# Performance work log

Hardware: AMD Instinct MI355X
Metric: run time of the kernel (lower is better)

Reference implementation:

```python
import jax, jax.numpy as jnp
import numpy as np

NUM_EMBEDDINGS = 4096
EMBEDDING_DIM = 256
COMMITMENT_COST = 0.25
N_INPUTS = 32768


def setup_inputs() -> dict:
    key = jax.random.key(0)
    k1, k2 = jax.random.split(key)
    inputs = jax.random.normal(k1, (N_INPUTS, EMBEDDING_DIM), dtype=jnp.float32)
    # embedding.weight initialized uniform(-1/K, 1/K)
    W = jax.random.uniform(k2, (NUM_EMBEDDINGS, EMBEDDING_DIM), dtype=jnp.float32,
                           minval=-1.0 / NUM_EMBEDDINGS, maxval=1.0 / NUM_EMBEDDINGS)
    return {"inputs": inputs, "W": W}


def reference(inputs, W):
    # pairwise squared L2 distances: [N, K]
    distances = (jnp.sum(inputs ** 2, axis=1, keepdims=True)
                 + jnp.sum(W ** 2, axis=1)
                 - 2.0 * inputs @ W.T)
    encoding_indices = jnp.argmin(distances, axis=1)           # [N]
    # one-hot scatter + matmul in torch == direct gather
    quantized = W[encoding_indices]                            # [N, D]

    e_latent_loss = jnp.mean((jax.lax.stop_gradient(quantized) - inputs) ** 2)
    q_latent_loss = jnp.mean((quantized - jax.lax.stop_gradient(inputs)) ** 2)
    loss = q_latent_loss + COMMITMENT_COST * e_latent_loss

    # straight-through estimator
    quantized_st = inputs + jax.lax.stop_gradient(quantized - inputs)

    # avg_probs = mean over N of one-hot encodings == normalized counts
    counts = jnp.zeros((NUM_EMBEDDINGS,), dtype=jnp.float32).at[encoding_indices].add(1.0)
    avg_probs = counts / inputs.shape[0]
    perplexity = jnp.exp(-jnp.sum(avg_probs * jnp.log(avg_probs + 1e-10)))

    return (loss, quantized_st, perplexity)
```

## Files before the change

### kernel.cpp

```cpp
#include <hip/hip_runtime.h>
#include <hip/hip_bf16.h>

#define M_IN  32768
#define K_EMB 4096
#define D_DIM 256

#define BM 256
#define BN 256
#define BK 32

#define WS_HWSQ   0
#define WS_PACKS  16384
#define WS_COUNTS 278528
#define WS_LOSS   294912
#define WS_XSQ    295168

using f32x4  = __attribute__((ext_vector_type(4))) float;
using bf16x8 = __attribute__((ext_vector_type(8))) short;

#define GLL16(g, p) __builtin_amdgcn_global_load_lds( \
    (const __attribute__((address_space(1))) void*)(g), \
    (__attribute__((address_space(3))) void*)(p), 16, 0, 0)

__device__ __forceinline__ unsigned short bf16_rtn(float f) {
    __hip_bfloat16 h = __float2bfloat16(f);
    return *reinterpret_cast<unsigned short*>(&h);
}

__global__ __launch_bounds__(256) void convx_kernel(const float* __restrict__ X,
                                                    unsigned short* __restrict__ Xb,
                                                    float* __restrict__ xsq,
                                                    unsigned long long* __restrict__ packs)
{
    const int l  = threadIdx.x & 63;
    const int wv = threadIdx.x >> 6;
    const int n  = blockIdx.x * 4 + wv;
    float4 v = ((const float4*)(X + (size_t)n * D_DIM))[l];
    float s = v.x * v.x + v.y * v.y + v.z * v.z + v.w * v.w;
    union { unsigned short u[4]; uint2 q; } p;
    p.u[0] = bf16_rtn(v.x); p.u[1] = bf16_rtn(v.y);
    p.u[2] = bf16_rtn(v.z); p.u[3] = bf16_rtn(v.w);
    ((uint2*)(Xb + (size_t)n * D_DIM))[l] = p.q;
#pragma unroll
    for (int off = 32; off; off >>= 1) s += __shfl_xor(s, off);
    if (l == 0) { xsq[n] = s; packs[n] = ~0ull; }
}

__global__ __launch_bounds__(256) void convw_kernel(const float* __restrict__ W,
                                                    unsigned short* __restrict__ Wb,
                                                    float* __restrict__ hwsq,
                                                    int* __restrict__ counts,
                                                    float* __restrict__ loss_slots)
{
    const int l = threadIdx.x & 63;
    const int k = blockIdx.x * 4 + (threadIdx.x >> 6);
    const int g = blockIdx.x * 256 + threadIdx.x;
    if (g < K_EMB) counts[g] = 0;
    if (g < 64)    loss_slots[g] = 0.f;
    float4 v = ((const float4*)(W + (size_t)k * D_DIM))[l];
    float s = v.x * v.x + v.y * v.y + v.z * v.z + v.w * v.w;
    union { unsigned short u[4]; uint2 q; } p;
    p.u[0] = bf16_rtn(v.x); p.u[1] = bf16_rtn(v.y);
    p.u[2] = bf16_rtn(v.z); p.u[3] = bf16_rtn(v.w);
    ((uint2*)(Wb + (size_t)k * D_DIM))[l] = p.q;
#pragma unroll
    for (int off = 32; off; off >>= 1) s += __shfl_xor(s, off);
    if (l == 0) hwsq[k] = 0.5f * s;
}


#define STAGE_A(KT, S) { \
  _Pragma("unroll") \
  for (int j_ = 0; j_ < 2; ++j_) { \
    const int row_ = (j_*8 + w)*16 + (l >> 2); \
    const int ch_  = ((l & 3) ^ ((l >> 3) & 3)); \
    const unsigned short* src_ = Xb + (size_t)(m0 + row_) * D_DIM + (KT)*BK + ch_*8; \
    GLL16(src_, lds + (S)*32768 + (j_*8 + w)*1024); \
  } }

#define STAGE_B(KT, S) { \
  _Pragma("unroll") \
  for (int j_ = 0; j_ < 2; ++j_) { \
    const int row_ = (j_*8 + w)*16 + (l >> 2); \
    const int ch_  = ((l & 3) ^ ((l >> 3) & 3)); \
    const unsigned short* src_ = Wb + (size_t)(nbase + row_) * D_DIM + (KT)*BK + ch_*8; \
    GLL16(src_, lds + (S)*32768 + 16384 + (j_*8 + w)*1024); \
  } }

#define K_ITER(T, VM)                                                          \
  {                                                                            \
    asm volatile("s_waitcnt vmcnt(" #VM ")" ::: "memory");                     \
    __builtin_amdgcn_s_barrier();                                              \
    __builtin_amdgcn_sched_barrier(0);                                         \
    const char* As_ = (const char*)lds + ((T)&3)*32768;                        \
    const char* Bs_ = As_ + 16384;                                             \
    if ((T) < 5) STAGE_A((T)+3, ((T)+3)&3);                                    \
    bf16x8 bfr[4], af[4];                                                      \
    _Pragma("unroll")                                                          \
    for (int nj = 0; nj < 4; nj++)                                             \
      bfr[nj] = *(const bf16x8*)(Bs_ + (rbB + nj*16)*64 + cswz);               \
    _Pragma("unroll")                                                          \
    for (int mi = 0; mi < 4; mi++)                                             \
      af[mi] = *(const bf16x8*)(As_ + (rbA + mi*16)*64 + cswz);                \
    asm volatile("s_waitcnt lgkmcnt(0)" ::: "memory");                         \
    __builtin_amdgcn_sched_barrier(0);                                         \
    __builtin_amdgcn_s_setprio(1);                                             \
    _Pragma("unroll")                                                          \
    for (int mi = 0; mi < 4; mi++)                                             \
      _Pragma("unroll")                                                        \
      for (int nj = 0; nj < 4; nj++)                                           \
        acc[mi][nj] = __builtin_amdgcn_mfma_f32_16x16x32_bf16(                 \
            af[mi], bfr[nj], acc[mi][nj], 0, 0, 0);                            \
    __builtin_amdgcn_s_setprio(0);                                             \
    if ((T) < 5) STAGE_B((T)+3, ((T)+3)&3);                                    \
    _Pragma("unroll")                                                          \
    for (int mi = 0; mi < 4; mi++)                                             \
      af[mi] = *(const bf16x8*)(As_ + (rbA + 64 + mi*16)*64 + cswz);           \
    asm volatile("s_waitcnt lgkmcnt(0)" ::: "memory");                         \
    __builtin_amdgcn_sched_barrier(0);                                         \
    __builtin_amdgcn_s_setprio(1);                                             \
    _Pragma("unroll")                                                          \
    for (int mi = 0; mi < 4; mi++)                                             \
      _Pragma("unroll")                                                        \
      for (int nj = 0; nj < 4; nj++)                                           \
        acc[4+mi][nj] = __builtin_amdgcn_mfma_f32_16x16x32_bf16(               \
            af[mi], bfr[nj], acc[4+mi][nj], 0, 0, 0);                          \
    __builtin_amdgcn_s_setprio(0);                                             \
  }

__global__ __launch_bounds__(512, 2) void dist_kernel(const unsigned short* __restrict__ Xb,
                                                      const unsigned short* __restrict__ Wb,
                                                      const float* __restrict__ hwsq,
                                                      unsigned long long* __restrict__ packs)
{
    __shared__ char lds[131072];

    const int t = threadIdx.x;
    const int l = t & 63;
    const int w = t >> 6;
    const int wm = w >> 2, wn = w & 3;

    const int id  = blockIdx.x;
    const int swz = (id & 7) * 256 + (id >> 3);
    const int nb = swz & 15, mb = swz >> 4;
    const int m0 = mb * BM, nbase = nb * BN;

    const int rbA = wm * 128 + (l & 15);
    const int rbB = wn * 64  + (l & 15);
    const int cswz = ((l >> 4) * 16) ^ (((((l & 15)) >> 1) & 3) << 4);

    f32x4 acc[8][4];
#pragma unroll
    for (int mi = 0; mi < 8; mi++)
#pragma unroll
        for (int nj = 0; nj < 4; nj++) acc[mi][nj] = (f32x4){0.f, 0.f, 0.f, 0.f};

    STAGE_A(0, 0); STAGE_B(0, 0);
    STAGE_A(1, 1); STAGE_B(1, 1);
    STAGE_A(2, 2); STAGE_B(2, 2);

    K_ITER(0, 8)
    K_ITER(1, 8)
    K_ITER(2, 8)
    K_ITER(3, 8)
    K_ITER(4, 8)
    K_ITER(5, 8)
    K_ITER(6, 4)
    K_ITER(7, 0)

    unsigned long long* mlds = (unsigned long long*)lds;
    float hw[4];
#pragma unroll
    for (int nj = 0; nj < 4; nj++)
        hw[nj] = hwsq[nbase + wn * 64 + nj * 16 + (l & 15)];

#pragma unroll
    for (int mi = 0; mi < 8; mi++) {
#pragma unroll
        for (int r = 0; r < 4; r++) {
            float bv = 3.4e38f; int bi = 0;
#pragma unroll
            for (int nj = 0; nj < 4; nj++) {
                const float v = hw[nj] - acc[mi][nj][r];
                const int idx = nbase + wn * 64 + nj * 16 + (l & 15);
                if (v < bv) { bv = v; bi = idx; }
            }
            unsigned long long pk =
                ((unsigned long long)__float_as_uint(bv + 1.0f) << 32) | (unsigned)bi;
#pragma unroll
            for (int off = 1; off < 16; off <<= 1) {
                const unsigned long long o = __shfl_xor(pk, off);
                if (o < pk) pk = o;
            }
            if ((l & 15) == 0)
                mlds[(wm * 128 + mi * 16 + (l >> 4) * 4 + r) * 4 + wn] = pk;
        }
    }
    __syncthreads();
    if (t < BM) {
        unsigned long long p = mlds[t * 4];
#pragma unroll
        for (int q = 1; q < 4; q++) {
            const unsigned long long o = mlds[t * 4 + q];
            if (o < p) p = o;
        }
        atomicMin(&packs[m0 + t], p);
    }
}

__global__ __launch_bounds__(256) void merge_kernel(const float* __restrict__ W,
                                                    const unsigned long long* __restrict__ packs,
                                                    const float* __restrict__ xsq,
                                                    int* __restrict__ counts,
                                                    float* __restrict__ loss_slots,
                                                    char* __restrict__ outbase )
{
    const int l   = threadIdx.x & 63;
    const int wv  = threadIdx.x >> 6;
    const int n0w = blockIdx.x * 64 + wv * 16;

    const unsigned long long pk = packs[n0w + (l & 15)];
    const int pkl = (int)(unsigned)(pk & 0xffffffffull);

    if (l < 16) atomicAdd(&counts[pkl], 1);

    float ls = xsq[n0w + (l & 15)] + 2.0f * (__uint_as_float((unsigned)(pk >> 32)) - 1.0f);
#pragma unroll
    for (int off = 32; off; off >>= 1) ls += __shfl_xor(ls, off);
    if (l == 0) atomicAdd(&loss_slots[(blockIdx.x * 4 + wv) & 63], 0.25f * ls);

    float4 v[16];
#pragma unroll
    for (int r = 0; r < 16; r++) {
        const int idxr = __shfl(pkl, r);
        v[r] = ((const float4*)(W + (size_t)idxr * D_DIM))[l];
    }

#pragma unroll
    for (int r = 0; r < 16; r++) {
        char* bp = outbase + (size_t)(n0w + r) * 1024;
        const float nx = __shfl_down(v[r].x, 1);
        const float ny = __shfl_down(v[r].y, 1);
        const float nz = __shfl_down(v[r].z, 1);
        if (l < 63)
            *(float4*)(bp + 12 + 16 * l) = make_float4(v[r].w, nx, ny, nz);
        if (l == 0) {
            ((float*)bp)[0] = v[r].x; ((float*)bp)[1] = v[r].y; ((float*)bp)[2] = v[r].z;
        }
        if (l == 63) ((float*)bp)[255] = v[r].w;
    }
}

__global__ __launch_bounds__(256) void finalize_kernel(const int* __restrict__ counts,
                                                       const float* __restrict__ loss_slots,
                                                       float* __restrict__ out)
{
    const int tid = threadIdx.x;
    float ent = 0.f;
    for (int k = tid; k < K_EMB; k += 256) {
        const float p = (float)counts[k] * (1.0f / (float)M_IN);
        ent += p * logf(p + 1e-10f);
    }
#pragma unroll
    for (int off = 32; off; off >>= 1) ent += __shfl_xor(ent, off);
    __shared__ float red[4];
    if ((tid & 63) == 0) red[tid >> 6] = ent;
    __syncthreads();
    if (tid == 0) {
        const float e = red[0] + red[1] + red[2] + red[3];
        float ls = 0.f;
        for (int i = 0; i < 64; i++) ls += loss_slots[i];
        out[0] = 1.25f * ls / ((float)M_IN * (float)D_DIM);
        out[1 + (size_t)M_IN * D_DIM] = expf(-e);
    }
}

extern "C" void kernel_launch(void* const* d_in, const int* in_sizes, int n_in,
                              void* d_out, int out_size, void* d_ws, size_t ws_size,
                              hipStream_t stream)
{
    const float* X = (const float*)d_in[0];
    const float* W = (const float*)d_in[1];
    float* out = (float*)d_out;
    char*  ws  = (char*)d_ws;

    float* hwsq               = (float*)(ws + WS_HWSQ);
    unsigned long long* packs = (unsigned long long*)(ws + WS_PACKS);
    int*   counts             = (int*)(ws + WS_COUNTS);
    float* loss_slots         = (float*)(ws + WS_LOSS);
    float* xsq                = (float*)(ws + WS_XSQ);

    unsigned short* Xb = (unsigned short*)((char*)d_out + 16);
    unsigned short* Wb = (unsigned short*)((char*)d_out + 16 + 16777216);

    convx_kernel<<<M_IN / 4, 256, 0, stream>>>(X, Xb, xsq, packs);
    convw_kernel<<<K_EMB / 4, 256, 0, stream>>>(W, Wb, hwsq, counts, loss_slots);
    dist_kernel<<<(M_IN / BM) * (K_EMB / BN), 512, 0, stream>>>(Xb, Wb, hwsq, packs);
    merge_kernel<<<M_IN / 64, 256, 0, stream>>>(W, packs, xsq, counts, loss_slots,
                                                (char*)d_out + 4);
    finalize_kernel<<<1, 256, 0, stream>>>(counts, loss_slots, out);
}
```

Baseline: 244.3 us.

## Keep codebook tile in registers and stream bf16-converted inputs through LDS

Restructures the distance GEMM so that each wave holds a 64-row slice of the bf16 codebook in registers for the whole kernel. Each block walks 1024 input rows, converting fp32 inputs to bf16 on the fly into a double-buffered swizzled LDS tile. This removes the separate input conversion kernel and its bf16 round trip through global memory, and the x-squared norm for the loss is now computed in the merge kernel. The trade-offs are heavy register pressure, only 256 blocks, and more global atomicMin traffic, since each row partial is issued per 16-lane group instead of being reduced in LDS first.

```diff
diff --git a/kernel.cpp b/kernel.cpp
--- a/kernel.cpp
+++ b/kernel.cpp
@@ -4,46 +4,18 @@
 #define M_IN  32768
 #define K_EMB 4096
 #define D_DIM 256
-
-#define BM 256
-#define BN 256
-#define BK 32
 
 #define WS_HWSQ   0
 #define WS_PACKS  16384
 #define WS_COUNTS 278528
 #define WS_LOSS   294912
-#define WS_XSQ    295168
 
 using f32x4  = __attribute__((ext_vector_type(4))) float;
 using bf16x8 = __attribute__((ext_vector_type(8))) short;
 
-#define GLL16(g, p) __builtin_amdgcn_global_load_lds( \
-    (const __attribute__((address_space(1))) void*)(g), \
-    (__attribute__((address_space(3))) void*)(p), 16, 0, 0)
-
-__device__ __forceinline__ unsigned short bf16_rtn(float f) {
+static __device__ __forceinline__ unsigned short bf16_rtn(float f) {
     __hip_bfloat16 h = __float2bfloat16(f);
     return *reinterpret_cast<unsigned short*>(&h);
-}
-
-__global__ __launch_bounds__(256) void convx_kernel(const float* __restrict__ X,
-                                                    unsigned short* __restrict__ Xb,
-                                                    float* __restrict__ xsq,
-                                                    unsigned long long* __restrict__ packs)
-{
-    const int l  = threadIdx.x & 63;
-    const int wv = threadIdx.x >> 6;
-    const int n  = blockIdx.x * 4 + wv;
-    float4 v = ((const float4*)(X + (size_t)n * D_DIM))[l];
-    float s = v.x * v.x + v.y * v.y + v.z * v.z + v.w * v.w;
-    union { unsigned short u[4]; uint2 q; } p;
-    p.u[0] = bf16_rtn(v.x); p.u[1] = bf16_rtn(v.y);
-    p.u[2] = bf16_rtn(v.z); p.u[3] = bf16_rtn(v.w);
-    ((uint2*)(Xb + (size_t)n * D_DIM))[l] = p.q;
-#pragma unroll
-    for (int off = 32; off; off >>= 1) s += __shfl_xor(s, off);
-    if (l == 0) { xsq[n] = s; packs[n] = ~0ull; }
 }
 
 __global__ __launch_bounds__(256) void convw_kernel(const float* __restrict__ W,
@@ -69,148 +41,165 @@
 }
 
 
-#define STAGE_A(KT, S) { \
-  _Pragma("unroll") \
-  for (int j_ = 0; j_ < 2; ++j_) { \
-    const int row_ = (j_*8 + w)*16 + (l >> 2); \
-    const int ch_  = ((l & 3) ^ ((l >> 3) & 3)); \
-    const unsigned short* src_ = Xb + (size_t)(m0 + row_) * D_DIM + (KT)*BK + ch_*8; \
-    GLL16(src_, lds + (S)*32768 + (j_*8 + w)*1024); \
+#define EPILOGUE(ACC, HALF) {                                                  \
+  _Pragma("unroll")                                                            \
+  for (int mih = 0; mih < 2; mih++) {                                          \
+    _Pragma("unroll")                                                          \
+    for (int r = 0; r < 4; r++) {                                              \
+      float bv = 3.4e38f; int bi = 0;                                          \
+      _Pragma("unroll")                                                        \
+      for (int nj = 0; nj < 4; nj++) {                                         \
+        const float v = hw[nj] - ACC[mih][nj][r];                              \
+        const int idx = nbase + nj*16 + (l & 15);                              \
+        if (v < bv) { bv = v; bi = idx; }                                      \
+      }                                                                        \
+      unsigned long long pk =                                                  \
+        ((unsigned long long)__float_as_uint(bv + 1.0f) << 32) | (unsigned)bi; \
+      _Pragma("unroll")                                                        \
+      for (int off = 1; off < 16; off <<= 1) {                                 \
+        const unsigned long long o = __shfl_xor(pk, off);                      \
+        if (o < pk) pk = o;                                                    \
+      }                                                                        \
+      if ((l & 15) == 0)                                                       \
+        atomicMin(&packs[m0 + t*64 + (HALF)*32 + mih*16 + (l>>4)*4 + r], pk);  \
+    }                                                                          \
   } }
 
-#define STAGE_B(KT, S) { \
-  _Pragma("unroll") \
-  for (int j_ = 0; j_ < 2; ++j_) { \
-    const int row_ = (j_*8 + w)*16 + (l >> 2); \
-    const int ch_  = ((l & 3) ^ ((l >> 3) & 3)); \
-    const unsigned short* src_ = Wb + (size_t)(nbase + row_) * D_DIM + (KT)*BK + ch_*8; \
-    GLL16(src_, lds + (S)*32768 + 16384 + (j_*8 + w)*1024); \
-  } }
-
-#define K_ITER(T, VM)                                                          \
-  {                                                                            \
-    asm volatile("s_waitcnt vmcnt(" #VM ")" ::: "memory");                     \
-    __builtin_amdgcn_s_barrier();                                              \
-    __builtin_amdgcn_sched_barrier(0);                                         \
-    const char* As_ = (const char*)lds + ((T)&3)*32768;                        \
-    const char* Bs_ = As_ + 16384;                                             \
-    if ((T) < 5) STAGE_A((T)+3, ((T)+3)&3);                                    \
-    bf16x8 bfr[4], af[4];                                                      \
-    _Pragma("unroll")                                                          \
-    for (int nj = 0; nj < 4; nj++)                                             \
-      bfr[nj] = *(const bf16x8*)(Bs_ + (rbB + nj*16)*64 + cswz);               \
-    _Pragma("unroll")                                                          \
-    for (int mi = 0; mi < 4; mi++)                                             \
-      af[mi] = *(const bf16x8*)(As_ + (rbA + mi*16)*64 + cswz);                \
-    asm volatile("s_waitcnt lgkmcnt(0)" ::: "memory");                         \
-    __builtin_amdgcn_sched_barrier(0);                                         \
-    __builtin_amdgcn_s_setprio(1);                                             \
-    _Pragma("unroll")                                                          \
-    for (int mi = 0; mi < 4; mi++)                                             \
-      _Pragma("unroll")                                                        \
-      for (int nj = 0; nj < 4; nj++)                                           \
-        acc[mi][nj] = __builtin_amdgcn_mfma_f32_16x16x32_bf16(                 \
-            af[mi], bfr[nj], acc[mi][nj], 0, 0, 0);                            \
-    __builtin_amdgcn_s_setprio(0);                                             \
-    if ((T) < 5) STAGE_B((T)+3, ((T)+3)&3);                                    \
-    _Pragma("unroll")                                                          \
-    for (int mi = 0; mi < 4; mi++)                                             \
-      af[mi] = *(const bf16x8*)(As_ + (rbA + 64 + mi*16)*64 + cswz);           \
-    asm volatile("s_waitcnt lgkmcnt(0)" ::: "memory");                         \
-    __builtin_amdgcn_sched_barrier(0);                                         \
-    __builtin_amdgcn_s_setprio(1);                                             \
-    _Pragma("unroll")                                                          \
-    for (int mi = 0; mi < 4; mi++)                                             \
-      _Pragma("unroll")                                                        \
-      for (int nj = 0; nj < 4; nj++)                                           \
-        acc[4+mi][nj] = __builtin_amdgcn_mfma_f32_16x16x32_bf16(               \
-            af[mi], bfr[nj], acc[4+mi][nj], 0, 0, 0);                          \
-    __builtin_amdgcn_s_setprio(0);                                             \
-  }
-
-__global__ __launch_bounds__(512, 2) void dist_kernel(const unsigned short* __restrict__ Xb,
+__global__ __launch_bounds__(512, 2) void dist_kernel(const float* __restrict__ X,
                                                       const unsigned short* __restrict__ Wb,
                                                       const float* __restrict__ hwsq,
                                                       unsigned long long* __restrict__ packs)
 {
-    __shared__ char lds[131072];
-
-    const int t = threadIdx.x;
-    const int l = t & 63;
-    const int w = t >> 6;
-    const int wm = w >> 2, wn = w & 3;
-
-    const int id  = blockIdx.x;
-    const int swz = (id & 7) * 256 + (id >> 3);
-    const int nb = swz & 15, mb = swz >> 4;
-    const int m0 = mb * BM, nbase = nb * BN;
-
-    const int rbA = wm * 128 + (l & 15);
-    const int rbB = wn * 64  + (l & 15);
-    const int cswz = ((l >> 4) * 16) ^ (((((l & 15)) >> 1) & 3) << 4);
-
-    f32x4 acc[8][4];
-#pragma unroll
-    for (int mi = 0; mi < 8; mi++)
-#pragma unroll
-        for (int nj = 0; nj < 4; nj++) acc[mi][nj] = (f32x4){0.f, 0.f, 0.f, 0.f};
-
-    STAGE_A(0, 0); STAGE_B(0, 0);
-    STAGE_A(1, 1); STAGE_B(1, 1);
-    STAGE_A(2, 2); STAGE_B(2, 2);
-
-    K_ITER(0, 8)
-    K_ITER(1, 8)
-    K_ITER(2, 8)
-    K_ITER(3, 8)
-    K_ITER(4, 8)
-    K_ITER(5, 8)
-    K_ITER(6, 4)
-    K_ITER(7, 0)
-
-    unsigned long long* mlds = (unsigned long long*)lds;
+    __shared__ char lds[65536];
+
+    const int tid = threadIdx.x;
+    const int l = tid & 63;
+    const int w = tid >> 6;
+
+    const int bid    = blockIdx.x;
+    const int nb     = (bid >> 3) & 7;
+    const int mchunk = (bid & 7) + ((bid >> 6) << 3);
+    const int m0     = mchunk * 1024;
+    const int nbase  = nb * 512 + w * 64;
+
+    bf16x8 bq[8][4];
+#pragma unroll
+    for (int kk = 0; kk < 8; kk++)
+#pragma unroll
+        for (int nj = 0; nj < 4; nj++) {
+            const int row = nbase + nj * 16 + (l & 15);
+            bq[kk][nj] = ((const bf16x8*)(Wb + (size_t)row * D_DIM))[kk * 4 + (l >> 4)];
+        }
+
     float hw[4];
 #pragma unroll
-    for (int nj = 0; nj < 4; nj++)
-        hw[nj] = hwsq[nbase + wn * 64 + nj * 16 + (l & 15)];
-
-#pragma unroll
-    for (int mi = 0; mi < 8; mi++) {
-#pragma unroll
-        for (int r = 0; r < 4; r++) {
-            float bv = 3.4e38f; int bi = 0;
-#pragma unroll
-            for (int nj = 0; nj < 4; nj++) {
-                const float v = hw[nj] - acc[mi][nj][r];
-                const int idx = nbase + wn * 64 + nj * 16 + (l & 15);
-                if (v < bv) { bv = v; bi = idx; }
-            }
-            unsigned long long pk =
-                ((unsigned long long)__float_as_uint(bv + 1.0f) << 32) | (unsigned)bi;
-#pragma unroll
-            for (int off = 1; off < 16; off <<= 1) {
-                const unsigned long long o = __shfl_xor(pk, off);
-                if (o < pk) pk = o;
-            }
-            if ((l & 15) == 0)
-                mlds[(wm * 128 + mi * 16 + (l >> 4) * 4 + r) * 4 + wn] = pk;
-        }
-    }
-    __syncthreads();
-    if (t < BM) {
-        unsigned long long p = mlds[t * 4];
-#pragma unroll
-        for (int q = 1; q < 4; q++) {
-            const unsigned long long o = mlds[t * 4 + q];
-            if (o < p) p = o;
-        }
-        atomicMin(&packs[m0 + t], p);
-    }
-}
-
-__global__ __launch_bounds__(256) void merge_kernel(const float* __restrict__ W,
+    for (int nj = 0; nj < 4; nj++) hw[nj] = hwsq[nbase + nj * 16 + (l & 15)];
+
+    const int rl   = w * 2 + (l >> 5);
+    const int gsrc = (l & 31) ^ (rl & 7);
+    const int Gb   = (w * 64 + l) * 16;
+
+    {
+        float4 xr[8];
+#pragma unroll
+        for (int j = 0; j < 4; j++) {
+            const float* src = X + (size_t)(m0 + j * 16 + rl) * D_DIM + gsrc * 8;
+            xr[2 * j]     = ((const float4*)src)[0];
+            xr[2 * j + 1] = ((const float4*)src)[1];
+        }
+#pragma unroll
+        for (int j = 0; j < 4; j++) {
+            union { unsigned short u[8]; bf16x8 v; } pw;
+            pw.u[0] = bf16_rtn(xr[2*j].x);   pw.u[1] = bf16_rtn(xr[2*j].y);
+            pw.u[2] = bf16_rtn(xr[2*j].z);   pw.u[3] = bf16_rtn(xr[2*j].w);
+            pw.u[4] = bf16_rtn(xr[2*j+1].x); pw.u[5] = bf16_rtn(xr[2*j+1].y);
+            pw.u[6] = bf16_rtn(xr[2*j+1].z); pw.u[7] = bf16_rtn(xr[2*j+1].w);
+            *(bf16x8*)(&lds[j * 8192 + Gb]) = pw.v;
+        }
+    }
+
+    for (int t = 0; t < 16; t++) {
+        __syncthreads();
+        const char* buf  = &lds[(t & 1) * 32768];
+        char*       nbuf = &lds[((t + 1) & 1) * 32768];
+
+        float4 xr[8];
+        if (t < 15) {
+#pragma unroll
+            for (int j = 0; j < 4; j++) {
+                const float* src = X + (size_t)(m0 + (t + 1) * 64 + j * 16 + rl) * D_DIM + gsrc * 8;
+                xr[2 * j]     = ((const float4*)src)[0];
+                xr[2 * j + 1] = ((const float4*)src)[1];
+            }
+        }
+
+        f32x4 acc0[2][4];
+#pragma unroll
+        for (int mih = 0; mih < 2; mih++)
+#pragma unroll
+            for (int nj = 0; nj < 4; nj++) acc0[mih][nj] = (f32x4){0.f, 0.f, 0.f, 0.f};
+#pragma unroll
+        for (int kk = 0; kk < 8; kk++) {
+            bf16x8 af[2];
+#pragma unroll
+            for (int mih = 0; mih < 2; mih++) {
+                const int r = mih * 16 + (l & 15);
+                const int perm = (kk * 4 + (l >> 4)) ^ (l & 7);
+                af[mih] = *(const bf16x8*)(buf + r * 512 + perm * 16);
+            }
+            __builtin_amdgcn_s_setprio(1);
+#pragma unroll
+            for (int mih = 0; mih < 2; mih++)
+#pragma unroll
+                for (int nj = 0; nj < 4; nj++)
+                    acc0[mih][nj] = __builtin_amdgcn_mfma_f32_16x16x32_bf16(
+                        af[mih], bq[kk][nj], acc0[mih][nj], 0, 0, 0);
+            __builtin_amdgcn_s_setprio(0);
+        }
+        EPILOGUE(acc0, 0)
+
+        f32x4 acc1[2][4];
+#pragma unroll
+        for (int mih = 0; mih < 2; mih++)
+#pragma unroll
+            for (int nj = 0; nj < 4; nj++) acc1[mih][nj] = (f32x4){0.f, 0.f, 0.f, 0.f};
+#pragma unroll
+        for (int kk = 0; kk < 8; kk++) {
+            bf16x8 af[2];
+#pragma unroll
+            for (int mih = 0; mih < 2; mih++) {
+                const int r = 32 + mih * 16 + (l & 15);
+                const int perm = (kk * 4 + (l >> 4)) ^ (l & 7);
+                af[mih] = *(const bf16x8*)(buf + r * 512 + perm * 16);
+            }
+            __builtin_amdgcn_s_setprio(1);
+#pragma unroll
+            for (int mih = 0; mih < 2; mih++)
+#pragma unroll
+                for (int nj = 0; nj < 4; nj++)
+                    acc1[mih][nj] = __builtin_amdgcn_mfma_f32_16x16x32_bf16(
+                        af[mih], bq[kk][nj], acc1[mih][nj], 0, 0, 0);
+            __builtin_amdgcn_s_setprio(0);
+        }
+
+        if (t < 15) {
+#pragma unroll
+            for (int j = 0; j < 4; j++) {
+                union { unsigned short u[8]; bf16x8 v; } pw;
+                pw.u[0] = bf16_rtn(xr[2*j].x);   pw.u[1] = bf16_rtn(xr[2*j].y);
+                pw.u[2] = bf16_rtn(xr[2*j].z);   pw.u[3] = bf16_rtn(xr[2*j].w);
+                pw.u[4] = bf16_rtn(xr[2*j+1].x); pw.u[5] = bf16_rtn(xr[2*j+1].y);
+                pw.u[6] = bf16_rtn(xr[2*j+1].z); pw.u[7] = bf16_rtn(xr[2*j+1].w);
+                *(bf16x8*)(&nbuf[j * 8192 + Gb]) = pw.v;
+            }
+        }
+        EPILOGUE(acc1, 1)
+    }
+}
+
+__global__ __launch_bounds__(256) void merge_kernel(const float* __restrict__ X,
+                                                    const float* __restrict__ W,
                                                     const unsigned long long* __restrict__ packs,
-                                                    const float* __restrict__ xsq,
                                                     int* __restrict__ counts,
                                                     float* __restrict__ loss_slots,
                                                     char* __restrict__ outbase )
@@ -224,10 +213,16 @@
 
     if (l < 16) atomicAdd(&counts[pkl], 1);
 
-    float ls = xsq[n0w + (l & 15)] + 2.0f * (__uint_as_float((unsigned)(pk >> 32)) - 1.0f);
-#pragma unroll
-    for (int off = 32; off; off >>= 1) ls += __shfl_xor(ls, off);
-    if (l == 0) atomicAdd(&loss_slots[(blockIdx.x * 4 + wv) & 63], 0.25f * ls);
+    float xacc = 0.f;
+#pragma unroll
+    for (int r = 0; r < 16; r++) {
+        const float4 xv = ((const float4*)(X + (size_t)(n0w + r) * D_DIM))[l];
+        xacc = fmaf(xv.x, xv.x, fmaf(xv.y, xv.y, fmaf(xv.z, xv.z, fmaf(xv.w, xv.w, xacc))));
+    }
+    float comb = xacc + ((l < 16) ? 2.0f * (__uint_as_float((unsigned)(pk >> 32)) - 1.0f) : 0.f);
+#pragma unroll
+    for (int off = 32; off; off >>= 1) comb += __shfl_xor(comb, off);
+    if (l == 0) atomicAdd(&loss_slots[(blockIdx.x * 4 + wv) & 63], comb);
 
     float4 v[16];
 #pragma unroll
@@ -235,7 +230,6 @@
         const int idxr = __shfl(pkl, r);
         v[r] = ((const float4*)(W + (size_t)idxr * D_DIM))[l];
     }
-
 #pragma unroll
     for (int r = 0; r < 16; r++) {
         char* bp = outbase + (size_t)(n0w + r) * 1024;
@@ -288,15 +282,14 @@
     unsigned long long* packs = (unsigned long long*)(ws + WS_PACKS);
     int*   counts             = (int*)(ws + WS_COUNTS);
     float* loss_slots         = (float*)(ws + WS_LOSS);
-    float* xsq                = (float*)(ws + WS_XSQ);
-
-    unsigned short* Xb = (unsigned short*)((char*)d_out + 16);
-    unsigned short* Wb = (unsigned short*)((char*)d_out + 16 + 16777216);
-
-    convx_kernel<<<M_IN / 4, 256, 0, stream>>>(X, Xb, xsq, packs);
+
+    unsigned short* Wb = (unsigned short*)((char*)d_out + 4096);
+
+    hipMemsetAsync(packs, 0xFF, 262144, stream);
+
     convw_kernel<<<K_EMB / 4, 256, 0, stream>>>(W, Wb, hwsq, counts, loss_slots);
-    dist_kernel<<<(M_IN / BM) * (K_EMB / BN), 512, 0, stream>>>(Xb, Wb, hwsq, packs);
-    merge_kernel<<<M_IN / 64, 256, 0, stream>>>(W, packs, xsq, counts, loss_slots,
+    dist_kernel<<<256, 512, 0, stream>>>(X, Wb, hwsq, packs);
+    merge_kernel<<<M_IN / 64, 256, 0, stream>>>(X, W, packs, counts, loss_slots,
                                                 (char*)d_out + 4);
     finalize_kernel<<<1, 256, 0, stream>>>(counts, loss_slots, out);
 }
```

After: 299.9 us. +22.8%, slower.
